# Performance work log

Measured on AMD Instinct MI355X. Metric: run time of the kernel, lower is better.

## Reference

```python
import jax, jax.numpy as jnp
import numpy as np

# Module hyperparameters (from init_kwargs)
NUM_NEURONS = 16384
BATCH = 2048  # processed sequentially, sharing neuron state
V_TH0 = 1.0
V_RESET = 0.0
TAU = 20.0
DT = 1.0
ETA = 0.1
NOISE_STD = 0.1
MIN_TH = 0.5
MAX_TH = 2.0
USE_ADAPTIVE = True
STOCHASTIC = True


def setup_inputs() -> dict:
    key = jax.random.key(0)
    k1, k2 = jax.random.split(key)
    input_current = jax.random.normal(k1, (BATCH, NUM_NEURONS), dtype=jnp.float32)
    # stochastic membrane noise, pre-sampled for determinism
    noise = NOISE_STD * jax.random.normal(k2, (BATCH, NUM_NEURONS), dtype=jnp.float32)
    if not STOCHASTIC:
        noise = jnp.zeros_like(noise)
    return {"input_current": input_current, "noise": noise}


def reference(input_current, noise):
    # Faithful to the torch wrapper: each batch row is fed through the SAME
    # LIFNeuronGroup sequentially, carrying membrane potential V and the
    # adaptive threshold V_th across rows -> lax.scan over the batch axis.
    n = input_current.shape[1]
    V0 = jnp.full((n,), V_RESET, dtype=jnp.float32)
    Vth0 = jnp.full((n,), V_TH0, dtype=jnp.float32)

    def step(carry, inp):
        V, Vth = carry
        I, nz = inp
        # leaky integration + noise injection (fused elementwise)
        V = V + (DT / TAU) * (I - V) + nz
        spikes = V >= Vth
        V = jnp.where(spikes, V_RESET, V)
        if USE_ADAPTIVE:
            Vth = jnp.clip(Vth + ETA * spikes.astype(jnp.float32), MIN_TH, MAX_TH)
        return (V, Vth), spikes.astype(jnp.float32)

    (_, _), out_spikes = jax.lax.scan(step, (V0, Vth0), (input_current, noise))
    return out_spikes  # [batch, num_neurons] binary float32
```

## Files before the change

kernel.cpp:

```cpp
#include <hip/hip_runtime.h>


constexpr int N = 16384;
constexpr int T = 2048;
constexpr int U = 4;
constexpr int D = 8;
constexpr int C = T / U;
constexpr int MAIN = C - D;

__global__
__attribute__((amdgpu_flat_work_group_size(64, 64)))
__attribute__((amdgpu_waves_per_eu(1, 1)))
void TorchLIFNeuronGroup_85152021610615_kernel(const float* __restrict__ I,
                                               const float* __restrict__ Z,
                                               float* __restrict__ O) {
    #pragma clang fp contract(off)
    const int n = blockIdx.x * 64 + threadIdx.x;
    const float* ip = I + n;
    const float* zp = Z + n;
    float* op = O + n;

    float V   = 0.0f;
    float Vth = 1.0f;

    float bi[D][U], bz[D][U];

    #pragma unroll
    for (int d = 0; d < D; ++d) {
        #pragma unroll
        for (int u = 0; u < U; ++u) {
            bi[d][u] = __builtin_nontemporal_load(ip + (size_t)(d * U + u) * N);
            bz[d][u] = __builtin_nontemporal_load(zp + (size_t)(d * U + u) * N);
        }
    }

    int t = 0;
    for (int sc = 0; sc < MAIN; sc += D) {
        #pragma unroll
        for (int d = 0; d < D; ++d) {
            #pragma unroll
            for (int u = 0; u < U; ++u) {
                float dd = bi[d][u] - V;
                float v1 = V + 0.05f * dd;
                float v2 = v1 + bz[d][u];
                bool  s  = (v2 >= Vth);
                V = s ? 0.0f : v2;
                float nth = fminf(fmaxf(Vth + 0.1f, 0.5f), 2.0f);
                Vth = s ? nth : Vth;
                __builtin_nontemporal_store(s ? 1.0f : 0.0f,
                                            op + (size_t)(t + u) * N);
            }
            #pragma unroll
            for (int u = 0; u < U; ++u) {
                bi[d][u] = __builtin_nontemporal_load(ip + (size_t)(t + D * U + u) * N);
                bz[d][u] = __builtin_nontemporal_load(zp + (size_t)(t + D * U + u) * N);
            }
            __builtin_amdgcn_sched_barrier(0);
            t += U;
        }
    }

    #pragma unroll
    for (int d = 0; d < D; ++d) {
        #pragma unroll
        for (int u = 0; u < U; ++u) {
            float dd = bi[d][u] - V;
            float v1 = V + 0.05f * dd;
            float v2 = v1 + bz[d][u];
            bool  s  = (v2 >= Vth);
            V = s ? 0.0f : v2;
            float nth = fminf(fmaxf(Vth + 0.1f, 0.5f), 2.0f);
            Vth = s ? nth : Vth;
            __builtin_nontemporal_store(s ? 1.0f : 0.0f,
                                        op + (size_t)(t + u) * N);
        }
        t += U;
    }
}

extern "C" void kernel_launch(void* const* d_in, const int* in_sizes, int n_in,
                              void* d_out, int out_size, void* d_ws, size_t ws_size,
                              hipStream_t stream) {
    const float* input_current = (const float*)d_in[0];
    const float* noise         = (const float*)d_in[1];
    float* out                 = (float*)d_out;

    TorchLIFNeuronGroup_85152021610615_kernel<<<N / 64, 64, 0, stream>>>(
        input_current, noise, out);
}
```

Measured before the change: 324.1 us.

## Stream inputs through an LDS ring via global_load_lds with vectorized spike stores

Replaces the register-held prefetch buffers with a 16-slot LDS ring filled by direct global-to-LDS 16-byte DMA loads, keeping 14 chunks (56 timesteps) in flight. Each lane now loads 4 contiguous floats per DMA instead of scalar loads. Spikes are staged through a small LDS buffer so each lane can issue one 16-byte nontemporal store per 4 timesteps. Hand-tuned s_waitcnt vmcnt values order the pipeline. The aim is to hide DRAM latency in this low-occupancy, latency-bound sequential scan, at the cost of brittle manual counter accounting and extra LDS traffic.

```diff
diff --git a/kernel.cpp b/kernel.cpp
--- a/kernel.cpp
+++ b/kernel.cpp
@@ -4,78 +4,101 @@
 constexpr int N = 16384;
 constexpr int T = 2048;
 constexpr int U = 4;
-constexpr int D = 8;
 constexpr int C = T / U;
-constexpr int MAIN = C - D;
+constexpr int R = 16;
+constexpr int P = 14;
+
+static_assert(C == 512 && R == 16 && P <= R - 2, "schedule geometry");
+
+typedef float f4v __attribute__((ext_vector_type(4)));
+
+__device__ __forceinline__ void dma16(const float* g, float* l) {
+    __builtin_amdgcn_global_load_lds(
+        (const __attribute__((address_space(1))) void*)g,
+        (__attribute__((address_space(3))) void*)l, 16, 0, 0);
+}
+
+#define WAITV(K) asm volatile("s_waitcnt vmcnt(" #K ")" ::: "memory")
 
 __global__
 __attribute__((amdgpu_flat_work_group_size(64, 64)))
-__attribute__((amdgpu_waves_per_eu(1, 1)))
 void TorchLIFNeuronGroup_85152021610615_kernel(const float* __restrict__ I,
                                                const float* __restrict__ Z,
                                                float* __restrict__ O) {
     #pragma clang fp contract(off)
-    const int n = blockIdx.x * 64 + threadIdx.x;
-    const float* ip = I + n;
-    const float* zp = Z + n;
-    float* op = O + n;
+    __shared__ __align__(16) float ring[R][2][U][64];
+    __shared__ __align__(16) float sbuf[U][64];
+
+    const int lane = threadIdx.x;
+    const int g    = lane >> 4;
+    const int c4   = (lane & 15) << 2;
+    const size_t laneOff = (size_t)g * N + c4;
+
+    const float* ipfx = I + (size_t)blockIdx.x * 64 + laneOff;
+    const float* zpfx = Z + (size_t)blockIdx.x * 64 + laneOff;
+    float*       opfx = O + (size_t)blockIdx.x * 64 + laneOff;
 
     float V   = 0.0f;
     float Vth = 1.0f;
 
-    float bi[D][U], bz[D][U];
-
     #pragma unroll
-    for (int d = 0; d < D; ++d) {
-        #pragma unroll
-        for (int u = 0; u < U; ++u) {
-            bi[d][u] = __builtin_nontemporal_load(ip + (size_t)(d * U + u) * N);
-            bz[d][u] = __builtin_nontemporal_load(zp + (size_t)(d * U + u) * N);
-        }
+    for (int c = 0; c < P; ++c) {
+        dma16(ipfx + (size_t)(c * U) * N, &ring[c][0][0][0]);
+        dma16(zpfx + (size_t)(c * U) * N, &ring[c][1][0][0]);
     }
 
     int t = 0;
-    for (int sc = 0; sc < MAIN; sc += D) {
-        #pragma unroll
-        for (int d = 0; d < D; ++d) {
-            #pragma unroll
-            for (int u = 0; u < U; ++u) {
-                float dd = bi[d][u] - V;
-                float v1 = V + 0.05f * dd;
-                float v2 = v1 + bz[d][u];
-                bool  s  = (v2 >= Vth);
-                V = s ? 0.0f : v2;
-                float nth = fminf(fmaxf(Vth + 0.1f, 0.5f), 2.0f);
-                Vth = s ? nth : Vth;
-                __builtin_nontemporal_store(s ? 1.0f : 0.0f,
-                                            op + (size_t)(t + u) * N);
-            }
-            #pragma unroll
-            for (int u = 0; u < U; ++u) {
-                bi[d][u] = __builtin_nontemporal_load(ip + (size_t)(t + D * U + u) * N);
-                bz[d][u] = __builtin_nontemporal_load(zp + (size_t)(t + D * U + u) * N);
-            }
-            __builtin_amdgcn_sched_barrier(0);
-            t += U;
-        }
+
+#define STAGE(d, K, PF)                                                       \
+    {                                                                         \
+        WAITV(K);                                                             \
+        _Pragma("unroll")                                                     \
+        for (int u = 0; u < U; ++u) {                                         \
+            float Iv = ring[d][0][u][lane];                                   \
+            float Zv = ring[d][1][u][lane];                                   \
+            float dd = Iv - V;                                                \
+            float v1 = V + 0.05f * dd;                            \
+            float v2 = v1 + Zv;                                               \
+            bool  s  = (v2 >= Vth);                                           \
+            V = s ? 0.0f : v2;                                                \
+            float nth = fminf(fmaxf(Vth + 0.1f, 0.5f), 2.0f);                 \
+            Vth = s ? nth : Vth;                                              \
+            sbuf[u][lane] = s ? 1.0f : 0.0f;                                  \
+        }                                                                     \
+        {                                                                     \
+            f4v sv = *reinterpret_cast<const f4v*>(&sbuf[g][c4]);             \
+            __builtin_nontemporal_store(                                      \
+                sv, reinterpret_cast<f4v*>(opfx + (size_t)t * N));            \
+        }                                                                     \
+        if (PF) {                                                             \
+            dma16(ipfx + (size_t)(t + P * U) * N,                             \
+                  &ring[(d + P) & (R - 1)][0][0][0]);                         \
+            dma16(zpfx + (size_t)(t + P * U) * N,                             \
+                  &ring[(d + P) & (R - 1)][1][0][0]);                         \
+        }                                                                     \
+        __builtin_amdgcn_sched_barrier(0);                                    \
+        t += U;                                                               \
     }
 
-    #pragma unroll
-    for (int d = 0; d < D; ++d) {
-        #pragma unroll
-        for (int u = 0; u < U; ++u) {
-            float dd = bi[d][u] - V;
-            float v1 = V + 0.05f * dd;
-            float v2 = v1 + bz[d][u];
-            bool  s  = (v2 >= Vth);
-            V = s ? 0.0f : v2;
-            float nth = fminf(fmaxf(Vth + 0.1f, 0.5f), 2.0f);
-            Vth = s ? nth : Vth;
-            __builtin_nontemporal_store(s ? 1.0f : 0.0f,
-                                        op + (size_t)(t + u) * N);
-        }
-        t += U;
+    STAGE(0, 26, 1)  STAGE(1, 27, 1)  STAGE(2, 28, 1)  STAGE(3, 29, 1)
+    STAGE(4, 30, 1)  STAGE(5, 31, 1)  STAGE(6, 32, 1)  STAGE(7, 33, 1)
+    STAGE(8, 34, 1)  STAGE(9, 35, 1)  STAGE(10, 36, 1) STAGE(11, 37, 1)
+    STAGE(12, 38, 1) STAGE(13, 39, 1) STAGE(14, 39, 1) STAGE(15, 39, 1)
+
+    for (int it = 1; it <= 30; ++it) {
+        STAGE(0, 39, 1)  STAGE(1, 39, 1)  STAGE(2, 39, 1)  STAGE(3, 39, 1)
+        STAGE(4, 39, 1)  STAGE(5, 39, 1)  STAGE(6, 39, 1)  STAGE(7, 39, 1)
+        STAGE(8, 39, 1)  STAGE(9, 39, 1)  STAGE(10, 39, 1) STAGE(11, 39, 1)
+        STAGE(12, 39, 1) STAGE(13, 39, 1) STAGE(14, 39, 1) STAGE(15, 39, 1)
     }
+
+    STAGE(0, 39, 1)  STAGE(1, 39, 1)
+    STAGE(2, 39, 0)  STAGE(3, 37, 0)  STAGE(4, 35, 0)  STAGE(5, 33, 0)
+    STAGE(6, 31, 0)  STAGE(7, 29, 0)  STAGE(8, 27, 0)  STAGE(9, 25, 0)
+    STAGE(10, 23, 0) STAGE(11, 21, 0) STAGE(12, 19, 0) STAGE(13, 17, 0)
+    STAGE(14, 15, 0) STAGE(15, 13, 0)
+
+#undef STAGE
 }
 
 extern "C" void kernel_launch(void* const* d_in, const int* in_sizes, int n_in,
```

Result: faster. 313.1 us (-3.4%).

## Warp-specialize LIF scan into loader, storer and compute waves via LDS

Applied to the files above, without the earlier changes.

Each block now has four waves. Two waves prefetch input and noise with 16-byte vector loads into double-buffered shared memory, one wave performs the serial scan reading from LDS and writing spikes to LDS, and one wave drains spikes to global memory with vector stores. The aim is to take global memory latency and address work off the serial dependency chain and to use wider memory transactions. In exchange, every section adds a block barrier and LDS traffic, which may stall the compute wave.

```diff
diff --git a/kernel.cpp b/kernel.cpp
--- a/kernel.cpp
+++ b/kernel.cpp
@@ -1,80 +1,138 @@
 #include <hip/hip_runtime.h>
 
 
-constexpr int N = 16384;
-constexpr int T = 2048;
-constexpr int U = 4;
-constexpr int D = 8;
-constexpr int C = T / U;
-constexpr int MAIN = C - D;
+constexpr int N  = 16384;
+constexpr int T  = 2048;
+constexpr int U  = 4;
+constexpr int CH = T / U;
+constexpr int S  = 8;
+constexpr int NSEC = CH / S;
+
+static_assert(NSEC % 4 == 0, "j-unroll of 4 needs NSEC % 4 == 0");
+
+typedef float f4v __attribute__((ext_vector_type(4)));
+
+#define BAR() do {                                                            \
+    asm volatile("s_waitcnt lgkmcnt(0)" ::: "memory");                        \
+    __builtin_amdgcn_s_barrier();                                             \
+    __builtin_amdgcn_sched_barrier(0);                                        \
+} while (0)
 
 __global__
-__attribute__((amdgpu_flat_work_group_size(64, 64)))
-__attribute__((amdgpu_waves_per_eu(1, 1)))
+__attribute__((amdgpu_flat_work_group_size(256, 256)))
 void TorchLIFNeuronGroup_85152021610615_kernel(const float* __restrict__ I,
                                                const float* __restrict__ Z,
                                                float* __restrict__ O) {
     #pragma clang fp contract(off)
-    const int n = blockIdx.x * 64 + threadIdx.x;
-    const float* ip = I + n;
-    const float* zp = Z + n;
-    float* op = O + n;
+    __shared__ __align__(16) float IZ[2][2][S][U][64];
+    __shared__ __align__(16) float SB[2][S][U][64];
+
+    const int w    = threadIdx.x >> 6;
+    const int lane = threadIdx.x & 63;
+    const int g    = lane >> 4;
+    const int c4   = (lane & 15) << 2;
+    const size_t laneOff = (size_t)g * N + c4;
+    const size_t nbase   = (size_t)blockIdx.x * 64;
+
+    const float* pfx  = (w == 0 ? I : Z) + nbase + laneOff;
+    float*       opfx = O + nbase + laneOff;
 
     float V   = 0.0f;
     float Vth = 1.0f;
+    f4v rg[4][S];
+    f4v sv[S];
 
-    float bi[D][U], bz[D][U];
+    if (w <= 1) {
+        #pragma unroll
+        for (int s = 0; s < 3; ++s)
+            #pragma unroll
+            for (int c = 0; c < S; ++c)
+                rg[s][c] = __builtin_nontemporal_load(
+                    reinterpret_cast<const f4v*>(
+                        pfx + (size_t)(U * (S * s + c)) * N));
+        #pragma unroll
+        for (int c = 0; c < S; ++c)
+            *reinterpret_cast<f4v*>(&IZ[0][w][c][0][0] + lane * 4) = rg[0][c];
+    }
+    BAR();
 
-    #pragma unroll
-    for (int d = 0; d < D; ++d) {
+    #pragma clang loop unroll(disable)
+    for (int kb = 0; kb < NSEC / 4; ++kb) {
         #pragma unroll
-        for (int u = 0; u < U; ++u) {
-            bi[d][u] = __builtin_nontemporal_load(ip + (size_t)(d * U + u) * N);
-            bz[d][u] = __builtin_nontemporal_load(zp + (size_t)(d * U + u) * N);
+        for (int j = 0; j < 4; ++j) {
+            const int k = kb * 4 + j;
+            if (w <= 1) {
+                if (k <= NSEC - 2) {
+                    #pragma unroll
+                    for (int c = 0; c < S; ++c)
+                        *reinterpret_cast<f4v*>(
+                            &IZ[(j + 1) & 1][w][c][0][0] + lane * 4) =
+                            rg[(j + 1) & 3][c];
+                }
+                if (k <= NSEC - 4) {
+                    #pragma unroll
+                    for (int c = 0; c < S; ++c)
+                        rg[(j + 3) & 3][c] = __builtin_nontemporal_load(
+                            reinterpret_cast<const f4v*>(
+                                pfx + (size_t)(U * (S * (k + 3) + c)) * N));
+                }
+            } else if (w == 2) {
+                if (k >= 1) {
+                    #pragma unroll
+                    for (int c = 0; c < S; ++c)
+                        sv[c] = *reinterpret_cast<const f4v*>(
+                            &SB[(j + 1) & 1][c][0][0] + lane * 4);
+                    #pragma unroll
+                    for (int c = 0; c < S; ++c)
+                        __builtin_nontemporal_store(sv[c],
+                            reinterpret_cast<f4v*>(
+                                opfx + (size_t)(U * (S * (k - 1) + c)) * N));
+                }
+            } else {
+                float ci[2][U], cz[2][U];
+                #pragma unroll
+                for (int u = 0; u < U; ++u) {
+                    ci[0][u] = IZ[j & 1][0][0][u][lane];
+                    cz[0][u] = IZ[j & 1][1][0][u][lane];
+                }
+                #pragma unroll
+                for (int c = 0; c < S; ++c) {
+                    if (c + 1 < S) {
+                        #pragma unroll
+                        for (int u = 0; u < U; ++u) {
+                            ci[(c + 1) & 1][u] = IZ[j & 1][0][c + 1][u][lane];
+                            cz[(c + 1) & 1][u] = IZ[j & 1][1][c + 1][u][lane];
+                        }
+                    }
+                    #pragma unroll
+                    for (int u = 0; u < U; ++u) {
+                        float Iv = ci[c & 1][u];
+                        float Zv = cz[c & 1][u];
+                        float dd = Iv - V;
+                        float v1 = V + 0.05f * dd;
+                        float v2 = v1 + Zv;
+                        bool  s  = (v2 >= Vth);
+                        V = s ? 0.0f : v2;
+                        float nth = fminf(fmaxf(Vth + 0.1f, 0.5f), 2.0f);
+                        Vth = s ? nth : Vth;
+                        SB[j & 1][c][u][lane] = s ? 1.0f : 0.0f;
+                    }
+                }
+            }
+            BAR();
         }
     }
 
-    int t = 0;
-    for (int sc = 0; sc < MAIN; sc += D) {
+    if (w == 2) {
         #pragma unroll
-        for (int d = 0; d < D; ++d) {
-            #pragma unroll
-            for (int u = 0; u < U; ++u) {
-                float dd = bi[d][u] - V;
-                float v1 = V + 0.05f * dd;
-                float v2 = v1 + bz[d][u];
-                bool  s  = (v2 >= Vth);
-                V = s ? 0.0f : v2;
-                float nth = fminf(fmaxf(Vth + 0.1f, 0.5f), 2.0f);
-                Vth = s ? nth : Vth;
-                __builtin_nontemporal_store(s ? 1.0f : 0.0f,
-                                            op + (size_t)(t + u) * N);
-            }
-            #pragma unroll
-            for (int u = 0; u < U; ++u) {
-                bi[d][u] = __builtin_nontemporal_load(ip + (size_t)(t + D * U + u) * N);
-                bz[d][u] = __builtin_nontemporal_load(zp + (size_t)(t + D * U + u) * N);
-            }
-            __builtin_amdgcn_sched_barrier(0);
-            t += U;
-        }
-    }
-
-    #pragma unroll
-    for (int d = 0; d < D; ++d) {
+        for (int c = 0; c < S; ++c)
+            sv[c] = *reinterpret_cast<const f4v*>(
+                &SB[1][c][0][0] + lane * 4);
         #pragma unroll
-        for (int u = 0; u < U; ++u) {
-            float dd = bi[d][u] - V;
-            float v1 = V + 0.05f * dd;
-            float v2 = v1 + bz[d][u];
-            bool  s  = (v2 >= Vth);
-            V = s ? 0.0f : v2;
-            float nth = fminf(fmaxf(Vth + 0.1f, 0.5f), 2.0f);
-            Vth = s ? nth : Vth;
-            __builtin_nontemporal_store(s ? 1.0f : 0.0f,
-                                        op + (size_t)(t + u) * N);
-        }
-        t += U;
+        for (int c = 0; c < S; ++c)
+            __builtin_nontemporal_store(sv[c],
+                reinterpret_cast<f4v*>(
+                    opfx + (size_t)(U * (S * (NSEC - 1) + c)) * N));
     }
 }
 
@@ -85,6 +143,6 @@
     const float* noise         = (const float*)d_in[1];
     float* out                 = (float*)d_out;
 
-    TorchLIFNeuronGroup_85152021610615_kernel<<<N / 64, 64, 0, stream>>>(
+    TorchLIFNeuronGroup_85152021610615_kernel<<<N / 64, 256, 0, stream>>>(
         input_current, noise, out);
 }
```

Result: faster. 289.4 us, median of 2 (-10.7%).
